# Kernel tuning notes

Hardware: AMD Instinct MI355X
Metric: run time of the kernel (lower is better)

## Reference

```python
import jax, jax.numpy as jnp
import numpy as np

N_NODES = 100000
N_EDGES = 1600000
NUM_FEATURES = 128
DIM = 64
NUM_GRAPHS = 64


def setup_inputs() -> dict:
    key = jax.random.key(0)
    ks = jax.random.split(key, 8)
    x = jax.random.normal(ks[0], (N_NODES, NUM_FEATURES), dtype=jnp.float32)
    edge_index = jax.random.randint(ks[1], (2, N_EDGES), 0, N_NODES, dtype=jnp.int64)
    batch = jnp.sort(jax.random.randint(ks[2], (N_NODES,), 0, NUM_GRAPHS, dtype=jnp.int64))
    s = 1.0 / np.sqrt(NUM_FEATURES)
    w_lin0 = jax.random.uniform(ks[3], (NUM_FEATURES, DIM), jnp.float32, -s, s)
    b_lin0 = jnp.zeros((DIM,), jnp.float32)
    s2 = 1.0 / np.sqrt(DIM)
    w0 = jax.random.uniform(ks[4], (DIM, DIM), jnp.float32, -s2, s2)
    w1 = jax.random.uniform(ks[5], (DIM, DIM), jnp.float32, -s2, s2)
    b_cheb = jnp.zeros((DIM,), jnp.float32)
    return {"x": x, "edge_index": edge_index, "batch": batch,
            "w_lin0": w_lin0, "b_lin0": b_lin0, "w0": w0, "w1": w1, "b_cheb": b_cheb}


def reference(x, edge_index, batch, w_lin0, b_lin0, w0, w1, b_cheb):
    # out = relu(lin0(x))
    out = jax.nn.relu(x @ w_lin0 + b_lin0)  # [N, DIM]

    src, dst = edge_index[0], edge_index[1]
    n = out.shape[0]
    # ChebConv K=2, sym normalization, lambda_max=2 (PyG default):
    # scaled Laplacian L_hat = L - I = -D^{-1/2} A D^{-1/2} (diagonal cancels to 0)
    deg = jax.ops.segment_sum(jnp.ones(src.shape, out.dtype), src, num_segments=n)
    dinv = jnp.where(deg > 0, 1.0 / jnp.sqrt(jnp.where(deg > 0, deg, 1.0)), 0.0)
    norm = -dinv[src] * dinv[dst]  # [E]

    tx0 = out
    # Tx_1 = L_hat @ x : gather source features, scale, scatter-add to targets
    tx1 = jax.ops.segment_sum(norm[:, None] * out[src], dst, num_segments=n)  # [N, DIM]

    h = jax.nn.relu(tx0 @ w0 + tx1 @ w1 + b_cheb)  # [N, DIM]

    pooled = jax.ops.segment_sum(h, batch, num_segments=NUM_GRAPHS)  # [G, DIM]
    return pooled, h
```

## Files before the change

### kernel.cpp

```cpp
#include <hip/hip_runtime.h>
#include <hip/hip_bf16.h>

#define N_NODES     100000
#define N_EDGES     1600000
#define NFEAT       128
#define DIM         64
#define NGRAPHS     64

#define SCAN_CHUNK  1024
#define SCAN_NB     ((N_NODES + SCAN_CHUNK - 1) / SCAN_CHUNK)

#define NCHUNK      8
#define CHUNK_NODES ((N_NODES + NCHUNK - 1) / NCHUNK)

__device__ __forceinline__ float bf2f(unsigned short u) {
    return __uint_as_float(((unsigned)u) << 16);
}
__device__ __forceinline__ unsigned short f2bf(float f) {
    unsigned u = __float_as_uint(f);
    u += 0x7fffu + ((u >> 16) & 1u);
    return (unsigned short)(u >> 16);
}

__global__ __launch_bounds__(256) void lin0_kernel(
    const float* __restrict__ x, const float* __restrict__ w,
    const float* __restrict__ b, unsigned short* __restrict__ tx0b)
{
    __shared__ float wl[NFEAT * DIM];
    for (int i = threadIdx.x; i < NFEAT * DIM; i += 256) wl[i] = w[i];
    __syncthreads();

    const int lane = threadIdx.x & 63;
    const int grp  = threadIdx.x >> 6;
    const int ROWS_PER_GROUP = 8;
    int r0 = blockIdx.x * (4 * ROWS_PER_GROUP) + grp * ROWS_PER_GROUP;
    const float bv = b[lane];

    for (int i = 0; i < ROWS_PER_GROUP; ++i) {
        int r = r0 + i;
        if (r >= N_NODES) break;
        float acc = bv;
        const float4* xr = (const float4*)(x + (size_t)r * NFEAT);
#pragma unroll
        for (int k4 = 0; k4 < NFEAT / 4; ++k4) {
            float4 xv = xr[k4];
            int k = k4 * 4;
            acc = fmaf(xv.x, wl[(k + 0) * DIM + lane], acc);
            acc = fmaf(xv.y, wl[(k + 1) * DIM + lane], acc);
            acc = fmaf(xv.z, wl[(k + 2) * DIM + lane], acc);
            acc = fmaf(xv.w, wl[(k + 3) * DIM + lane], acc);
        }
        tx0b[(size_t)r * DIM + lane] = f2bf(fmaxf(acc, 0.0f));
    }
}

__global__ __launch_bounds__(256) void hist_kernel(
    const int* __restrict__ ei, int* __restrict__ deg_src, int* __restrict__ cnt_dst)
{
    int e = blockIdx.x * 256 + threadIdx.x;
    if (e < N_EDGES) {
        atomicAdd(&deg_src[ei[e]], 1);
        atomicAdd(&cnt_dst[ei[N_EDGES + e]], 1);
    }
}

__global__ __launch_bounds__(256) void scan1_kernel(
    const int* __restrict__ cnt, int* __restrict__ local_scan, int* __restrict__ block_sums)
{
    __shared__ int wsum[4];
    int t = threadIdx.x;
    int idx = blockIdx.x * SCAN_CHUNK + t * 4;
    int v0 = (idx + 0 < N_NODES) ? cnt[idx + 0] : 0;
    int v1 = (idx + 1 < N_NODES) ? cnt[idx + 1] : 0;
    int v2 = (idx + 2 < N_NODES) ? cnt[idx + 2] : 0;
    int v3 = (idx + 3 < N_NODES) ? cnt[idx + 3] : 0;
    int tsum = v0 + v1 + v2 + v3;

    int lane = t & 63, wv = t >> 6;
    int x = tsum;
#pragma unroll
    for (int off = 1; off < 64; off <<= 1) {
        int y = __shfl_up(x, off, 64);
        if (lane >= off) x += y;
    }
    if (lane == 63) wsum[wv] = x;
    __syncthreads();
    int wbase = 0;
    for (int w = 0; w < wv; ++w) wbase += wsum[w];

    int excl = wbase + x - tsum;
    if (idx + 0 < N_NODES) local_scan[idx + 0] = excl; excl += v0;
    if (idx + 1 < N_NODES) local_scan[idx + 1] = excl; excl += v1;
    if (idx + 2 < N_NODES) local_scan[idx + 2] = excl; excl += v2;
    if (idx + 3 < N_NODES) local_scan[idx + 3] = excl;

    if (t == 255) block_sums[blockIdx.x] = wbase + x;
}

__global__ __launch_bounds__(256) void scan2_kernel(int* __restrict__ block_sums, int nb)
{
    __shared__ int wsum[4];
    int t = threadIdx.x;
    int v = (t < nb) ? block_sums[t] : 0;
    int lane = t & 63, wv = t >> 6;
    int x = v;
#pragma unroll
    for (int off = 1; off < 64; off <<= 1) {
        int y = __shfl_up(x, off, 64);
        if (lane >= off) x += y;
    }
    if (lane == 63) wsum[wv] = x;
    __syncthreads();
    int wbase = 0;
    for (int w = 0; w < wv; ++w) wbase += wsum[w];
    if (t < nb) block_sums[t] = wbase + x - v;
}

__global__ __launch_bounds__(256) void scan3_kernel(
    const int* __restrict__ local_scan, const int* __restrict__ block_sums,
    int* __restrict__ offs, int* __restrict__ cursor,
    const int* __restrict__ deg_src, float* __restrict__ dinv)
{
    int base = blockIdx.x * SCAN_CHUNK;
    int add = block_sums[blockIdx.x];
    for (int i = threadIdx.x; i < SCAN_CHUNK; i += 256) {
        int idx = base + i;
        if (idx < N_NODES) {
            int v = local_scan[idx] + add;
            offs[idx]   = v;
            cursor[idx] = v;
            int dg = deg_src[idx];
            dinv[idx] = (dg > 0) ? rsqrtf((float)dg) : 0.0f;
        }
    }
    if (blockIdx.x == 0 && threadIdx.x == 0) offs[N_NODES] = N_EDGES;
}

__global__ __launch_bounds__(256) void csr_scatter_kernel(
    const int* __restrict__ ei, int* __restrict__ cursor, int* __restrict__ csr_src)
{
    const int stride = gridDim.x * 256;
    for (int c = 0; c < NCHUNK; ++c) {
        int lo = c * CHUNK_NODES;
        int hi = lo + CHUNK_NODES;
        for (int e = blockIdx.x * 256 + threadIdx.x; e < N_EDGES; e += stride) {
            int d = ei[N_EDGES + e];
            if (d >= lo && d < hi) {
                int pos = atomicAdd(&cursor[d], 1);
                csr_src[pos] = ei[e];
            }
        }
    }
}

__global__ __launch_bounds__(256) void gather_kernel(
    const int* __restrict__ csr_src, const int* __restrict__ offs,
    const unsigned short* __restrict__ tx0b, const float* __restrict__ dinv,
    float* __restrict__ tx1)
{
    int node = blockIdx.x * 4 + (threadIdx.x >> 6);
    if (node >= N_NODES) return;
    int lane = threadIdx.x & 63;
    int sub  = lane >> 4;
    int q    = lane & 15;

    int beg = offs[node], end = offs[node + 1];
    float4 acc = make_float4(0.f, 0.f, 0.f, 0.f);
    for (int p = beg + sub; p < end; p += 4) {
        int s = csr_src[p];
        float ds = dinv[s];
        ushort4 v = *(const ushort4*)(tx0b + (size_t)s * DIM + q * 4);
        acc.x = fmaf(ds, bf2f(v.x), acc.x);
        acc.y = fmaf(ds, bf2f(v.y), acc.y);
        acc.z = fmaf(ds, bf2f(v.z), acc.z);
        acc.w = fmaf(ds, bf2f(v.w), acc.w);
    }
#pragma unroll
    for (int off = 16; off <= 32; off <<= 1) {
        acc.x += __shfl_xor(acc.x, off, 64);
        acc.y += __shfl_xor(acc.y, off, 64);
        acc.z += __shfl_xor(acc.z, off, 64);
        acc.w += __shfl_xor(acc.w, off, 64);
    }
    if (sub == 0) {
        float nd = -dinv[node];
        float4 r = make_float4(nd * acc.x, nd * acc.y, nd * acc.z, nd * acc.w);
        *(float4*)(tx1 + (size_t)node * DIM + q * 4) = r;
    }
}

__global__ __launch_bounds__(256) void cheb_kernel(
    const unsigned short* __restrict__ tx0b, const float* __restrict__ tx1,
    const float* __restrict__ w0, const float* __restrict__ w1,
    const float* __restrict__ b, const int* __restrict__ batch,
    float* __restrict__ pooled, float* __restrict__ h)
{
    __shared__ float w0l[DIM * DIM];
    __shared__ float w1l[DIM * DIM];
    for (int i = threadIdx.x; i < DIM * DIM; i += 256) {
        w0l[i] = w0[i];
        w1l[i] = w1[i];
    }
    __syncthreads();

    const int lane = threadIdx.x & 63;
    const int grp  = threadIdx.x >> 6;
    const int ROWS_PER_GROUP = 16;
    int r0 = blockIdx.x * 64 + grp * ROWS_PER_GROUP;
    const float bv = b[lane];

    float acc_pool = 0.0f;
    int cur_g = -1;

    for (int i = 0; i < ROWS_PER_GROUP; ++i) {
        int r = r0 + i;
        if (r >= N_NODES) break;
        float acc = bv;
        const ushort4* t0 = (const ushort4*)(tx0b + (size_t)r * DIM);
        const float4*  t1 = (const float4*)(tx1 + (size_t)r * DIM);
#pragma unroll
        for (int k4 = 0; k4 < DIM / 4; ++k4) {
            ushort4 a = t0[k4];
            float4  c = t1[k4];
            int k = k4 * 4;
            acc = fmaf(bf2f(a.x), w0l[(k + 0) * DIM + lane], acc);
            acc = fmaf(bf2f(a.y), w0l[(k + 1) * DIM + lane], acc);
            acc = fmaf(bf2f(a.z), w0l[(k + 2) * DIM + lane], acc);
            acc = fmaf(bf2f(a.w), w0l[(k + 3) * DIM + lane], acc);
            acc = fmaf(c.x, w1l[(k + 0) * DIM + lane], acc);
            acc = fmaf(c.y, w1l[(k + 1) * DIM + lane], acc);
            acc = fmaf(c.z, w1l[(k + 2) * DIM + lane], acc);
            acc = fmaf(c.w, w1l[(k + 3) * DIM + lane], acc);
        }
        float hv = fmaxf(acc, 0.0f);
        h[(size_t)r * DIM + lane] = hv;

        int g = batch[r];
        if (g != cur_g) {
            if (cur_g >= 0) unsafeAtomicAdd(&pooled[cur_g * DIM + lane], acc_pool);
            cur_g = g;
            acc_pool = 0.0f;
        }
        acc_pool += hv;
    }
    if (cur_g >= 0) unsafeAtomicAdd(&pooled[cur_g * DIM + lane], acc_pool);
}

extern "C" void kernel_launch(void* const* d_in, const int* in_sizes, int n_in,
                              void* d_out, int out_size, void* d_ws, size_t ws_size,
                              hipStream_t stream)
{
    const float* x      = (const float*)d_in[0];
    const int*   ei     = (const int*)d_in[1];
    const int*   batch  = (const int*)d_in[2];
    const float* w_lin0 = (const float*)d_in[3];
    const float* b_lin0 = (const float*)d_in[4];
    const float* w0     = (const float*)d_in[5];
    const float* w1     = (const float*)d_in[6];
    const float* b_cheb = (const float*)d_in[7];

    float* pooled = (float*)d_out;
    float* h      = (float*)d_out + NGRAPHS * DIM;

    char* wp = (char*)d_ws;
    unsigned short* tx0b = (unsigned short*)wp; wp += (size_t)N_NODES * DIM * sizeof(unsigned short);
    float* tx1        = (float*)wp;  wp += (size_t)N_NODES * DIM * sizeof(float);
    float* dinv       = (float*)wp;  wp += (size_t)N_NODES * sizeof(float);
    int*   deg_src    = (int*)wp;    wp += (size_t)N_NODES * sizeof(int);
    int*   cnt_dst    = (int*)wp;    wp += (size_t)N_NODES * sizeof(int);
    int*   local_scan = (int*)wp;    wp += (size_t)N_NODES * sizeof(int);
    int*   offs       = (int*)wp;    wp += (size_t)(N_NODES + 1) * sizeof(int);
    int*   cursor     = (int*)wp;    wp += (size_t)N_NODES * sizeof(int);
    int*   block_sums = (int*)wp;    wp += 256 * sizeof(int);
    int*   csr_src    = (int*)wp;    wp += (size_t)N_EDGES * sizeof(int);

    hipMemsetAsync(deg_src, 0, (size_t)2 * N_NODES * sizeof(int), stream);
    hipMemsetAsync(pooled, 0, (size_t)NGRAPHS * DIM * sizeof(float), stream);

    lin0_kernel<<<(N_NODES + 31) / 32, 256, 0, stream>>>(x, w_lin0, b_lin0, tx0b);

    hist_kernel<<<(N_EDGES + 255) / 256, 256, 0, stream>>>(ei, deg_src, cnt_dst);

    scan1_kernel<<<SCAN_NB, 256, 0, stream>>>(cnt_dst, local_scan, block_sums);
    scan2_kernel<<<1, 256, 0, stream>>>(block_sums, SCAN_NB);
    scan3_kernel<<<SCAN_NB, 256, 0, stream>>>(local_scan, block_sums, offs, cursor,
                                              deg_src, dinv);

    csr_scatter_kernel<<<2048, 256, 0, stream>>>(ei, cursor, csr_src);

    gather_kernel<<<(N_NODES + 3) / 4, 256, 0, stream>>>(csr_src, offs, tx0b, dinv, tx1);

    cheb_kernel<<<(N_NODES + 63) / 64, 256, 0, stream>>>(tx0b, tx1, w0, w1, b_cheb,
                                                         batch, pooled, h);
}
```

Before: 561.8 us.

## Fuse lin0 with histogram, register-block rows in lin0/cheb, unroll gather

Merges the degree histogram into the lin0 launch as extra blocks so both run concurrently. lin0 and cheb kernels now compute 8 rows per wave at once, reusing each shared-memory weight load across rows. The gather loop is unrolled by two to keep more independent loads in flight. The histogram blocks reserve unused shared memory, and the larger per-thread register arrays may reduce occupancy.

Result: no change. 562.8 us (+0.2%).

```diff
diff --git a/kernel.cpp b/kernel.cpp
--- a/kernel.cpp
+++ b/kernel.cpp
@@ -13,6 +13,10 @@
 #define NCHUNK      8
 #define CHUNK_NODES ((N_NODES + NCHUNK - 1) / NCHUNK)
 
+#define LIN0_ROWS_PB 128
+#define NB_LIN   ((N_NODES + LIN0_ROWS_PB - 1) / LIN0_ROWS_PB)
+#define NB_HIST  2048
+
 __device__ __forceinline__ float bf2f(unsigned short u) {
     return __uint_as_float(((unsigned)u) << 16);
 }
@@ -22,45 +26,58 @@
     return (unsigned short)(u >> 16);
 }
 
-__global__ __launch_bounds__(256) void lin0_kernel(
+__global__ __launch_bounds__(256) void lin0_hist_kernel(
     const float* __restrict__ x, const float* __restrict__ w,
-    const float* __restrict__ b, unsigned short* __restrict__ tx0b)
+    const float* __restrict__ b, unsigned short* __restrict__ tx0b,
+    const int* __restrict__ ei, int* __restrict__ deg_src, int* __restrict__ cnt_dst)
 {
     __shared__ float wl[NFEAT * DIM];
+
+    if (blockIdx.x >= NB_LIN) {
+        const int stride = NB_HIST * 256;
+        for (int e = (blockIdx.x - NB_LIN) * 256 + threadIdx.x; e < N_EDGES; e += stride) {
+            atomicAdd(&deg_src[ei[e]], 1);
+            atomicAdd(&cnt_dst[ei[N_EDGES + e]], 1);
+        }
+        return;
+    }
+
     for (int i = threadIdx.x; i < NFEAT * DIM; i += 256) wl[i] = w[i];
     __syncthreads();
 
     const int lane = threadIdx.x & 63;
-    const int grp  = threadIdx.x >> 6;
-    const int ROWS_PER_GROUP = 8;
-    int r0 = blockIdx.x * (4 * ROWS_PER_GROUP) + grp * ROWS_PER_GROUP;
+    const int wv   = threadIdx.x >> 6;
+    const int wave_r0 = blockIdx.x * LIN0_ROWS_PB + wv * 32;
     const float bv = b[lane];
 
-    for (int i = 0; i < ROWS_PER_GROUP; ++i) {
-        int r = r0 + i;
-        if (r >= N_NODES) break;
-        float acc = bv;
-        const float4* xr = (const float4*)(x + (size_t)r * NFEAT);
-#pragma unroll
+    for (int it = 0; it < 4; ++it) {
+        int r0 = wave_r0 + it * 8;
+        if (r0 >= N_NODES) break;
+        float acc[8];
+#pragma unroll
+        for (int j = 0; j < 8; ++j) acc[j] = bv;
+
         for (int k4 = 0; k4 < NFEAT / 4; ++k4) {
-            float4 xv = xr[k4];
-            int k = k4 * 4;
-            acc = fmaf(xv.x, wl[(k + 0) * DIM + lane], acc);
-            acc = fmaf(xv.y, wl[(k + 1) * DIM + lane], acc);
-            acc = fmaf(xv.z, wl[(k + 2) * DIM + lane], acc);
-            acc = fmaf(xv.w, wl[(k + 3) * DIM + lane], acc);
-        }
-        tx0b[(size_t)r * DIM + lane] = f2bf(fmaxf(acc, 0.0f));
-    }
-}
-
-__global__ __launch_bounds__(256) void hist_kernel(
-    const int* __restrict__ ei, int* __restrict__ deg_src, int* __restrict__ cnt_dst)
-{
-    int e = blockIdx.x * 256 + threadIdx.x;
-    if (e < N_EDGES) {
-        atomicAdd(&deg_src[ei[e]], 1);
-        atomicAdd(&cnt_dst[ei[N_EDGES + e]], 1);
+            const int k = k4 * 4;
+            float4 xv[8];
+#pragma unroll
+            for (int j = 0; j < 8; ++j)
+                xv[j] = *(const float4*)(x + (size_t)(r0 + j) * NFEAT + k);
+            float w0v = wl[(k + 0) * DIM + lane];
+            float w1v = wl[(k + 1) * DIM + lane];
+            float w2v = wl[(k + 2) * DIM + lane];
+            float w3v = wl[(k + 3) * DIM + lane];
+#pragma unroll
+            for (int j = 0; j < 8; ++j) {
+                acc[j] = fmaf(xv[j].x, w0v, acc[j]);
+                acc[j] = fmaf(xv[j].y, w1v, acc[j]);
+                acc[j] = fmaf(xv[j].z, w2v, acc[j]);
+                acc[j] = fmaf(xv[j].w, w3v, acc[j]);
+            }
+        }
+#pragma unroll
+        for (int j = 0; j < 8; ++j)
+            tx0b[(size_t)(r0 + j) * DIM + lane] = f2bf(fmaxf(acc[j], 0.0f));
     }
 }
 
@@ -166,7 +183,24 @@
 
     int beg = offs[node], end = offs[node + 1];
     float4 acc = make_float4(0.f, 0.f, 0.f, 0.f);
-    for (int p = beg + sub; p < end; p += 4) {
+    int p = beg + sub;
+    for (; p + 4 < end; p += 8) {
+        int s0 = csr_src[p];
+        int s1 = csr_src[p + 4];
+        float d0 = dinv[s0];
+        float d1 = dinv[s1];
+        ushort4 v0 = *(const ushort4*)(tx0b + (size_t)s0 * DIM + q * 4);
+        ushort4 v1 = *(const ushort4*)(tx0b + (size_t)s1 * DIM + q * 4);
+        acc.x = fmaf(d0, bf2f(v0.x), acc.x);
+        acc.y = fmaf(d0, bf2f(v0.y), acc.y);
+        acc.z = fmaf(d0, bf2f(v0.z), acc.z);
+        acc.w = fmaf(d0, bf2f(v0.w), acc.w);
+        acc.x = fmaf(d1, bf2f(v1.x), acc.x);
+        acc.y = fmaf(d1, bf2f(v1.y), acc.y);
+        acc.z = fmaf(d1, bf2f(v1.z), acc.z);
+        acc.w = fmaf(d1, bf2f(v1.w), acc.w);
+    }
+    if (p < end) {
         int s = csr_src[p];
         float ds = dinv[s];
         ushort4 v = *(const ushort4*)(tx0b + (size_t)s * DIM + q * 4);
@@ -204,44 +238,56 @@
     __syncthreads();
 
     const int lane = threadIdx.x & 63;
-    const int grp  = threadIdx.x >> 6;
-    const int ROWS_PER_GROUP = 16;
-    int r0 = blockIdx.x * 64 + grp * ROWS_PER_GROUP;
+    const int wv   = threadIdx.x >> 6;
+    const int wave_r0 = blockIdx.x * 128 + wv * 32;
     const float bv = b[lane];
 
     float acc_pool = 0.0f;
     int cur_g = -1;
 
-    for (int i = 0; i < ROWS_PER_GROUP; ++i) {
-        int r = r0 + i;
-        if (r >= N_NODES) break;
-        float acc = bv;
-        const ushort4* t0 = (const ushort4*)(tx0b + (size_t)r * DIM);
-        const float4*  t1 = (const float4*)(tx1 + (size_t)r * DIM);
-#pragma unroll
+    for (int it = 0; it < 4; ++it) {
+        int r0 = wave_r0 + it * 8;
+        if (r0 >= N_NODES) break;
+        float acc[8];
+#pragma unroll
+        for (int j = 0; j < 8; ++j) acc[j] = bv;
+
         for (int k4 = 0; k4 < DIM / 4; ++k4) {
-            ushort4 a = t0[k4];
-            float4  c = t1[k4];
-            int k = k4 * 4;
-            acc = fmaf(bf2f(a.x), w0l[(k + 0) * DIM + lane], acc);
-            acc = fmaf(bf2f(a.y), w0l[(k + 1) * DIM + lane], acc);
-            acc = fmaf(bf2f(a.z), w0l[(k + 2) * DIM + lane], acc);
-            acc = fmaf(bf2f(a.w), w0l[(k + 3) * DIM + lane], acc);
-            acc = fmaf(c.x, w1l[(k + 0) * DIM + lane], acc);
-            acc = fmaf(c.y, w1l[(k + 1) * DIM + lane], acc);
-            acc = fmaf(c.z, w1l[(k + 2) * DIM + lane], acc);
-            acc = fmaf(c.w, w1l[(k + 3) * DIM + lane], acc);
-        }
-        float hv = fmaxf(acc, 0.0f);
-        h[(size_t)r * DIM + lane] = hv;
-
-        int g = batch[r];
-        if (g != cur_g) {
-            if (cur_g >= 0) unsafeAtomicAdd(&pooled[cur_g * DIM + lane], acc_pool);
-            cur_g = g;
-            acc_pool = 0.0f;
-        }
-        acc_pool += hv;
+            const int k = k4 * 4;
+            float a0 = w0l[(k + 0) * DIM + lane];
+            float a1 = w0l[(k + 1) * DIM + lane];
+            float a2 = w0l[(k + 2) * DIM + lane];
+            float a3 = w0l[(k + 3) * DIM + lane];
+            float c0 = w1l[(k + 0) * DIM + lane];
+            float c1 = w1l[(k + 1) * DIM + lane];
+            float c2 = w1l[(k + 2) * DIM + lane];
+            float c3 = w1l[(k + 3) * DIM + lane];
+#pragma unroll
+            for (int j = 0; j < 8; ++j) {
+                ushort4 t0 = *(const ushort4*)(tx0b + (size_t)(r0 + j) * DIM + k);
+                float4  t1 = *(const float4*) (tx1  + (size_t)(r0 + j) * DIM + k);
+                acc[j] = fmaf(bf2f(t0.x), a0, acc[j]);
+                acc[j] = fmaf(bf2f(t0.y), a1, acc[j]);
+                acc[j] = fmaf(bf2f(t0.z), a2, acc[j]);
+                acc[j] = fmaf(bf2f(t0.w), a3, acc[j]);
+                acc[j] = fmaf(t1.x, c0, acc[j]);
+                acc[j] = fmaf(t1.y, c1, acc[j]);
+                acc[j] = fmaf(t1.z, c2, acc[j]);
+                acc[j] = fmaf(t1.w, c3, acc[j]);
+            }
+        }
+#pragma unroll
+        for (int j = 0; j < 8; ++j) {
+            float hv = fmaxf(acc[j], 0.0f);
+            h[(size_t)(r0 + j) * DIM + lane] = hv;
+            int g = batch[r0 + j];
+            if (g != cur_g) {
+                if (cur_g >= 0) unsafeAtomicAdd(&pooled[cur_g * DIM + lane], acc_pool);
+                cur_g = g;
+                acc_pool = 0.0f;
+            }
+            acc_pool += hv;
+        }
     }
     if (cur_g >= 0) unsafeAtomicAdd(&pooled[cur_g * DIM + lane], acc_pool);
 }
@@ -277,9 +323,8 @@
     hipMemsetAsync(deg_src, 0, (size_t)2 * N_NODES * sizeof(int), stream);
     hipMemsetAsync(pooled, 0, (size_t)NGRAPHS * DIM * sizeof(float), stream);
 
-    lin0_kernel<<<(N_NODES + 31) / 32, 256, 0, stream>>>(x, w_lin0, b_lin0, tx0b);
-
-    hist_kernel<<<(N_EDGES + 255) / 256, 256, 0, stream>>>(ei, deg_src, cnt_dst);
+    lin0_hist_kernel<<<NB_LIN + NB_HIST, 256, 0, stream>>>(x, w_lin0, b_lin0, tx0b,
+                                                           ei, deg_src, cnt_dst);
 
     scan1_kernel<<<SCAN_NB, 256, 0, stream>>>(cnt_dst, local_scan, block_sums);
     scan2_kernel<<<1, 256, 0, stream>>>(block_sums, SCAN_NB);
@@ -290,6 +335,6 @@
 
     gather_kernel<<<(N_NODES + 3) / 4, 256, 0, stream>>>(csr_src, offs, tx0b, dinv, tx1);
 
-    cheb_kernel<<<(N_NODES + 63) / 64, 256, 0, stream>>>(tx0b, tx1, w0, w1, b_cheb,
-                                                         batch, pooled, h);
-}
+    cheb_kernel<<<(N_NODES + 127) / 128, 256, 0, stream>>>(tx0b, tx1, w0, w1, b_cheb,
+                                                           batch, pooled, h);
+}
```
